# Performance work log

Hardware: AMD Instinct MI355X
Metric: run time of the kernel (lower is better)

## Reference

```python
import jax, jax.numpy as jnp
import numpy as np

N, K, D = 65536, 4096, 512
EPS_NORM = 1e-12
EPS_LOG = 1e-10


def _l2norm(x):
    # F.normalize(dim=-1): x / max(||x||, eps)
    n = jnp.sqrt(jnp.sum(x * x, axis=-1, keepdims=True))
    return x / jnp.maximum(n, EPS_NORM)


def setup_inputs() -> dict:
    key = jax.random.key(0)
    k1, k2, k3 = jax.random.split(key, 3)
    z_e = jax.random.normal(k1, (N, D), dtype=jnp.float32)
    embeddings = jax.random.normal(k2, (K, D), dtype=jnp.float32)
    logit_scale = jnp.ones((1,), dtype=jnp.float32) * 10.0
    residual_weight = jnp.asarray(0.3, dtype=jnp.float32)
    return {"z_e": z_e, "embeddings": embeddings,
            "logit_scale": logit_scale, "residual_weight": residual_weight}


def reference(z_e, embeddings, logit_scale, residual_weight):
    # cosine-similarity routing logits: [N, K]
    z_e_norm = _l2norm(z_e)
    emb_norm = _l2norm(embeddings)
    logits = logit_scale * jnp.einsum('nd,kd->nk', z_e_norm, emb_norm)

    # eval path (not training / not kmeans-initialized): hard argmax + gather
    indices = jnp.argmax(logits, axis=-1)          # [N] int
    z_q_pure = embeddings[indices]                 # [N, D]

    # learnable residual blend
    alpha = jax.nn.sigmoid(residual_weight)
    z_q = alpha * z_q_pure + (1.0 - alpha) * z_e

    # codebook usage perplexity
    probs = jax.nn.softmax(logits, axis=-1)        # [N, K]
    avg_probs = jnp.mean(probs, axis=0)            # [K]
    perplexity = jnp.exp(-jnp.sum(avg_probs * jnp.log(avg_probs + EPS_LOG)))

    return (z_q, indices, perplexity, alpha)
```

## Files before the change

### kernel.cpp

```cpp
#include <hip/hip_runtime.h>
#include <cstdint>
#include <cstddef>

#define N_ROWS 65536
#define K_CODES 4096
#define DIM 512
#define ND_OUT ((size_t)N_ROWS * DIM)

typedef __attribute__((ext_vector_type(8))) short  short8v;
typedef __attribute__((ext_vector_type(4))) float  f32x4;

#define WS_PACKED   0u
#define WS_SSUM     524288u
#define WS_AVGP     786432u
#define WS_ARN      802816u
#define WS_BRN      1064960u
#define WS_PLANES   2097152ull
#define SZ_APLANE   67108864ull
#define SZ_BPLANE   4194304ull
#define NEED_B      (WS_PLANES + 2*SZ_APLANE + 2*SZ_BPLANE)

#define PE_AH 0
#define PE_AL 33554432
#define PE_BH 67108864
#define PE_BL 69206016

#define GLOAD_LDS16(gsrc, ldst) \
  __builtin_amdgcn_global_load_lds((const __attribute__((address_space(1))) void*)(gsrc), \
                                   (__attribute__((address_space(3))) void*)(ldst), 16, 0, 0)

__device__ inline unsigned long long pack_max(float v, unsigned idx) {
    unsigned u = __float_as_uint(v);
    u = (u & 0x80000000u) ? ~u : (u | 0x80000000u);
    return ((unsigned long long)u << 32) | (unsigned)(~idx);
}

__device__ inline ushort bf16rn(float f) {
    unsigned u = __float_as_uint(f);
    u += 0x7FFFu + ((u >> 16) & 1u);
    return (ushort)(u >> 16);
}
__device__ inline float bf16f(ushort h) { return __uint_as_float((unsigned)h << 16); }


__global__ __launch_bounds__(256) void rownorm_kernel(const float* __restrict__ x,
                                                      float* __restrict__ out,
                                                      const float* __restrict__ scale_ptr) {
    int lane = threadIdx.x & 63;
    int row  = blockIdx.x * 4 + (threadIdx.x >> 6);
    const float4* x4 = reinterpret_cast<const float4*>(x) + (size_t)row * (DIM / 4);
    float4 v0 = x4[lane];
    float4 v1 = x4[64 + lane];
    float s = v0.x*v0.x + v0.y*v0.y + v0.z*v0.z + v0.w*v0.w
            + v1.x*v1.x + v1.y*v1.y + v1.z*v1.z + v1.w*v1.w;
#pragma unroll
    for (int off = 32; off; off >>= 1) s += __shfl_xor(s, off);
    if (lane == 0) {
        float scale = scale_ptr ? scale_ptr[0] : 1.0f;
        out[row] = scale / fmaxf(sqrtf(s), 1e-12f);
    }
}

__global__ __launch_bounds__(256) void split_bf16(const float* __restrict__ x,
                                                  ushort* __restrict__ hi,
                                                  ushort* __restrict__ lo, int n4) {
    int i = blockIdx.x * 256 + threadIdx.x;
    if (i >= n4) return;
    float4 v = reinterpret_cast<const float4*>(x)[i];
    ushort4 h, l;
    h.x = bf16rn(v.x); l.x = bf16rn(v.x - bf16f(h.x));
    h.y = bf16rn(v.y); l.y = bf16rn(v.y - bf16f(h.y));
    h.z = bf16rn(v.z); l.z = bf16rn(v.z - bf16f(h.z));
    h.w = bf16rn(v.w); l.w = bf16rn(v.w - bf16f(h.w));
    reinterpret_cast<ushort4*>(hi)[i] = h;
    reinterpret_cast<ushort4*>(lo)[i] = l;
}

template <int EPI, int TERMS>
__global__ __launch_bounds__(512, 2) void mfma2(
        const ushort* __restrict__ planes,
        const float* __restrict__ arn, const float* __restrict__ brn,
        unsigned long long* __restrict__ packed, float* __restrict__ ssum,
        float* __restrict__ avgp) {
    constexpr int BUFSZ = (TERMS == 4) ? 65536 : 32768;
    constexpr int BHOFF = (TERMS == 4) ? 32768 : 16384;
    constexpr int NST   = (TERMS == 4) ? 8 : 4;
    __shared__ __align__(16) char buf0[BUFSZ];
    __shared__ __align__(16) char buf1[BUFSZ];

    const int tid  = threadIdx.x;
    const int lane = tid & 63;
    const int wavei = __builtin_amdgcn_readfirstlane(tid >> 6);
    const int wr = wavei >> 1, wc = wavei & 1;
    const int r16 = lane & 15, kg = lane >> 4;

    const int orig = blockIdx.x;
    const int swz  = (orig & 7) * 512 + (orig >> 3);
    const int row0 = (swz >> 4) * 256, col0 = (swz & 15) * 256;

    const ushort* gsrc[NST];
    int ldsu[NST];
#pragma unroll
    for (int j = 0; j < NST; ++j) {
        int u = wavei * NST + j;
        int p = u >> 4, rb = u & 15;
        int pe, g0;
        if constexpr (TERMS == 4) {
            pe = (p == 0) ? PE_AH : (p == 1) ? PE_AL : (p == 2) ? PE_BH : PE_BL;
            g0 = (p < 2) ? row0 : col0;
        } else {
            pe = (p == 0) ? PE_AH : PE_BH;
            g0 = (p == 0) ? row0 : col0;
        }
        gsrc[j] = planes + pe + (size_t)(g0 + rb * 16 + r16) * DIM + kg * 8;
        ldsu[j] = u * 1024;
    }

    f32x4 acc[4][8];
#pragma unroll
    for (int m = 0; m < 4; ++m)
#pragma unroll
        for (int n = 0; n < 8; ++n) acc[m][n] = f32x4{0.f, 0.f, 0.f, 0.f};

#define MFMA_STEP(CUR, NXT, KT)                                                       \
    {                                                                                  \
        if ((KT) + 1 < 16) {                                                           \
            _Pragma("unroll")                                                          \
            for (int j = 0; j < NST; ++j)                                              \
                GLOAD_LDS16(gsrc[j] + ((KT) + 1) * 32, (char*)(NXT) + ldsu[j]);        \
        }                                                                              \
        short8v ah[4], al[4];                                                          \
        _Pragma("unroll")                                                              \
        for (int m = 0; m < 4; ++m) {                                                  \
            ah[m] = *(const short8v*)((CUR) + (wr * 4 + m) * 1024 + lane * 16);        \
            if constexpr (TERMS == 4)                                                  \
                al[m] = *(const short8v*)((CUR) + 16384 + (wr * 4 + m) * 1024 + lane * 16); \
        }                                                                              \
        __builtin_amdgcn_s_setprio(1);                                                 \
        _Pragma("unroll")                                                              \
        for (int nh = 0; nh < 2; ++nh) {                                               \
            short8v bh[4], bl[4];                                                      \
            _Pragma("unroll")                                                          \
            for (int n = 0; n < 4; ++n) {                                              \
                int nn = nh * 4 + n;                                                   \
                bh[n] = *(const short8v*)((CUR) + BHOFF + (wc * 8 + nn) * 1024 + lane * 16); \
                if constexpr (TERMS == 4)                                              \
                    bl[n] = *(const short8v*)((CUR) + 49152 + (wc * 8 + nn) * 1024 + lane * 16); \
            }                                                                          \
            _Pragma("unroll")                                                          \
            for (int m = 0; m < 4; ++m)                                                \
                _Pragma("unroll")                                                      \
                for (int n = 0; n < 4; ++n) {                                          \
                    int nn = nh * 4 + n;                                               \
                    acc[m][nn] = __builtin_amdgcn_mfma_f32_16x16x32_bf16(ah[m], bh[n], acc[m][nn], 0, 0, 0); \
                    if constexpr (TERMS == 4) {                                        \
                        acc[m][nn] = __builtin_amdgcn_mfma_f32_16x16x32_bf16(ah[m], bl[n], acc[m][nn], 0, 0, 0); \
                        acc[m][nn] = __builtin_amdgcn_mfma_f32_16x16x32_bf16(al[m], bh[n], acc[m][nn], 0, 0, 0); \
                        acc[m][nn] = __builtin_amdgcn_mfma_f32_16x16x32_bf16(al[m], bl[n], acc[m][nn], 0, 0, 0); \
                    }                                                                  \
                }                                                                      \
        }                                                                              \
        __builtin_amdgcn_s_setprio(0);                                                 \
        __syncthreads();                                                               \
    }

#pragma unroll
    for (int j = 0; j < NST; ++j)
        GLOAD_LDS16(gsrc[j], (char*)buf0 + ldsu[j]);
    __syncthreads();

#pragma unroll 1
    for (int kt = 0; kt < 16; kt += 2) {
        MFMA_STEP(buf0, buf1, kt);
        MFMA_STEP(buf1, buf0, kt + 1);
    }
#undef MFMA_STEP

    const int g = lane >> 4, c15 = lane & 15;
    float bc[8];
#pragma unroll
    for (int n = 0; n < 8; ++n) bc[n] = brn[col0 + wc * 128 + n * 16 + c15];

    if constexpr (EPI == 0) {
#pragma unroll
        for (int m = 0; m < 4; ++m)
#pragma unroll
            for (int rr = 0; rr < 4; ++rr) {
                const int grow = row0 + wr * 64 + m * 16 + g * 4 + rr;
                const float ar = arn[grow];
                float mx = -1e30f; int mi = 0; float se = 0.f;
#pragma unroll
                for (int n = 0; n < 8; ++n) {
                    float lg = acc[m][n][rr] * ar * bc[n];
                    int gcol = col0 + wc * 128 + n * 16 + c15;
                    se += __expf(lg);
                    if (lg > mx || (lg == mx && gcol < mi)) { mx = lg; mi = gcol; }
                }
#pragma unroll
                for (int off = 1; off < 16; off <<= 1) {
                    float om = __shfl_xor(mx, off, 16);
                    int   oi = __shfl_xor(mi, off, 16);
                    float os = __shfl_xor(se, off, 16);
                    se += os;
                    if (om > mx || (om == mx && oi < mi)) { mx = om; mi = oi; }
                }
                if (c15 == 0) {
                    atomicMax(packed + grow, pack_max(mx, (unsigned)mi));
                    atomicAdd(&ssum[grow], se);
                }
            }
    } else {
        float cp[8] = {0.f, 0.f, 0.f, 0.f, 0.f, 0.f, 0.f, 0.f};
#pragma unroll
        for (int m = 0; m < 4; ++m)
#pragma unroll
            for (int rr = 0; rr < 4; ++rr) {
                const int grow = row0 + wr * 64 + m * 16 + g * 4 + rr;
                const float ar = arn[grow];
                const float si = 1.0f / ssum[grow];
#pragma unroll
                for (int n = 0; n < 8; ++n)
                    cp[n] += __expf(acc[m][n][rr] * ar * bc[n]) * si;
            }
#pragma unroll
        for (int n = 0; n < 8; ++n) {
            cp[n] += __shfl_xor(cp[n], 16);
            cp[n] += __shfl_xor(cp[n], 32);
        }
        float* sm = (float*)buf0;
        if (g == 0) {
#pragma unroll
            for (int n = 0; n < 8; ++n) sm[wavei * 128 + n * 16 + c15] = cp[n];
        }
        __syncthreads();
        if (tid < 256) {
            int wcc = tid >> 7, j = tid & 127;
            float s = sm[(0 + wcc) * 128 + j] + sm[(2 + wcc) * 128 + j]
                    + sm[(4 + wcc) * 128 + j] + sm[(6 + wcc) * 128 + j];
            atomicAdd(&avgp[col0 + wcc * 128 + j], s);
        }
    }
}

template <int PASS>
__global__ __launch_bounds__(256) void gemm_pass(
        const float* __restrict__ A, const float* __restrict__ B,
        const float* __restrict__ arn, const float* __restrict__ brn,
        unsigned long long* __restrict__ packed, float* __restrict__ ssum,
        float* __restrict__ avgp) {
    __shared__ __align__(16) float As[16][132];
    __shared__ __align__(16) float Bs[16][132];
    const int tid = threadIdx.x;
    const int tr = tid >> 4, tc = tid & 15;
    const int row0 = blockIdx.y * 128, col0 = blockIdx.x * 128;

    float acc[8][8] = {};
    const float4* A4 = reinterpret_cast<const float4*>(A);
    const float4* B4 = reinterpret_cast<const float4*>(B);

    for (int d0 = 0; d0 < DIM; d0 += 16) {
#pragma unroll
        for (int l = 0; l < 2; ++l) {
            int q = tid + l * 256;
            int r = q >> 2, dq = q & 3;
            float4 av = A4[(size_t)(row0 + r) * (DIM / 4) + (d0 >> 2) + dq];
            float4 bv = B4[(size_t)(col0 + r) * (DIM / 4) + (d0 >> 2) + dq];
            As[dq*4+0][r] = av.x; As[dq*4+1][r] = av.y; As[dq*4+2][r] = av.z; As[dq*4+3][r] = av.w;
            Bs[dq*4+0][r] = bv.x; Bs[dq*4+1][r] = bv.y; Bs[dq*4+2][r] = bv.z; Bs[dq*4+3][r] = bv.w;
        }
        __syncthreads();
#pragma unroll
        for (int dd = 0; dd < 16; ++dd) {
            float4 a0 = *reinterpret_cast<const float4*>(&As[dd][tr * 4]);
            float4 a1 = *reinterpret_cast<const float4*>(&As[dd][64 + tr * 4]);
            float4 b0 = *reinterpret_cast<const float4*>(&Bs[dd][tc * 4]);
            float4 b1 = *reinterpret_cast<const float4*>(&Bs[dd][64 + tc * 4]);
            float av[8] = {a0.x, a0.y, a0.z, a0.w, a1.x, a1.y, a1.z, a1.w};
            float bv[8] = {b0.x, b0.y, b0.z, b0.w, b1.x, b1.y, b1.z, b1.w};
#pragma unroll
            for (int i = 0; i < 8; ++i)
#pragma unroll
                for (int j = 0; j < 8; ++j)
                    acc[i][j] = fmaf(av[i], bv[j], acc[i][j]);
        }
        __syncthreads();
    }

    int rows[8], cols[8];
    float ar[8], bcv[8];
#pragma unroll
    for (int i = 0; i < 8; ++i) {
        rows[i] = (i < 4) ? (tr * 4 + i) : (64 + tr * 4 + i - 4);
        ar[i] = arn[row0 + rows[i]];
    }
#pragma unroll
    for (int j = 0; j < 8; ++j) {
        cols[j] = (j < 4) ? (tc * 4 + j) : (64 + tc * 4 + j - 4);
        bcv[j] = brn[col0 + cols[j]];
    }

    if constexpr (PASS == 1) {
#pragma unroll
        for (int i = 0; i < 8; ++i) {
            float m = -1e30f; int mi = 0; float se = 0.0f;
#pragma unroll
            for (int j = 0; j < 8; ++j) {
                float l = acc[i][j] * ar[i] * bcv[j];
                int c = col0 + cols[j];
                if (l > m || (l == m && c < mi)) { m = l; mi = c; }
                se += expf(l);
            }
#pragma unroll
            for (int off = 1; off < 16; off <<= 1) {
                float om = __shfl_xor(m, off, 16);
                int   oi = __shfl_xor(mi, off, 16);
                float os = __shfl_xor(se, off, 16);
                se += os;
                if (om > m || (om == m && oi < mi)) { m = om; mi = oi; }
            }
            if (tc == 0) {
                int grow = row0 + rows[i];
                atomicMax(packed + grow, pack_max(m, (unsigned)mi));
                atomicAdd(&ssum[grow], se);
            }
        }
    } else {
        float sinv[8];
#pragma unroll
        for (int i = 0; i < 8; ++i) sinv[i] = 1.0f / ssum[row0 + rows[i]];
        float cp[8] = {};
#pragma unroll
        for (int i = 0; i < 8; ++i)
#pragma unroll
            for (int j = 0; j < 8; ++j)
                cp[j] += expf(acc[i][j] * ar[i] * bcv[j]) * sinv[i];
        __syncthreads();
        float* red = &As[0][0];
#pragma unroll
        for (int j = 0; j < 8; ++j) red[tr * 128 + cols[j]] = cp[j];
        __syncthreads();
        if (tid < 128) {
            float s = 0.0f;
#pragma unroll
            for (int t = 0; t < 16; ++t) s += red[t * 128 + tid];
            atomicAdd(&avgp[col0 + tid], s);
        }
    }
}

__global__ __launch_bounds__(256) void zq_kernel(const float* __restrict__ ze,
                                                 const float* __restrict__ emb,
                                                 const unsigned long long* __restrict__ packed,
                                                 const float* __restrict__ resw,
                                                 float* __restrict__ out) {
    int q = blockIdx.x * 256 + threadIdx.x;
    int n = q >> 7, d4 = q & 127;
    unsigned idx = ~(unsigned)(packed[n] & 0xFFFFFFFFull);
    float alpha = 1.0f / (1.0f + expf(-resw[0]));
    float4 e = reinterpret_cast<const float4*>(emb)[(size_t)idx * 128 + d4];
    float4 z = reinterpret_cast<const float4*>(ze)[(size_t)n * 128 + d4];
    float4 o;
    o.x = alpha * e.x + (1.0f - alpha) * z.x;
    o.y = alpha * e.y + (1.0f - alpha) * z.y;
    o.z = alpha * e.z + (1.0f - alpha) * z.z;
    o.w = alpha * e.w + (1.0f - alpha) * z.w;
    reinterpret_cast<float4*>(out)[(size_t)n * 128 + d4] = o;
    if (d4 == 0) out[ND_OUT + n] = (float)idx;
}

__global__ __launch_bounds__(256) void finalize_kernel(const float* __restrict__ avgp,
                                                       const float* __restrict__ resw,
                                                       float* __restrict__ out) {
    float acc = 0.0f;
    for (int k = threadIdx.x; k < K_CODES; k += 256) {
        float p = avgp[k] * (1.0f / (float)N_ROWS);
        acc += p * logf(p + 1e-10f);
    }
    __shared__ float red[4];
#pragma unroll
    for (int off = 32; off; off >>= 1) acc += __shfl_xor(acc, off);
    int lane = threadIdx.x & 63, wave = threadIdx.x >> 6;
    if (lane == 0) red[wave] = acc;
    __syncthreads();
    if (threadIdx.x == 0) {
        float s = red[0] + red[1] + red[2] + red[3];
        out[ND_OUT + N_ROWS]     = expf(-s);
        out[ND_OUT + N_ROWS + 1] = 1.0f / (1.0f + expf(-resw[0]));
    }
}

extern "C" void kernel_launch(void* const* d_in, const int* in_sizes, int n_in,
                              void* d_out, int out_size, void* d_ws, size_t ws_size,
                              hipStream_t stream) {
    const float* ze   = (const float*)d_in[0];
    const float* emb  = (const float*)d_in[1];
    const float* ls   = (const float*)d_in[2];
    const float* resw = (const float*)d_in[3];
    float* out = (float*)d_out;

    char* ws = (char*)d_ws;
    unsigned long long* packed = (unsigned long long*)(ws + WS_PACKED);
    float* ssum = (float*)(ws + WS_SSUM);
    float* avgp = (float*)(ws + WS_AVGP);
    float* arn  = (float*)(ws + WS_ARN);
    float* brn  = (float*)(ws + WS_BRN);

    hipMemsetAsync(d_ws, 0, 802816, stream);

    rownorm_kernel<<<N_ROWS / 4, 256, 0, stream>>>(ze, arn, ls);
    rownorm_kernel<<<K_CODES / 4, 256, 0, stream>>>(emb, brn, nullptr);

    if (ws_size >= NEED_B) {
        ushort* planes = (ushort*)(ws + WS_PLANES);
        split_bf16<<<(N_ROWS * DIM / 4) / 256, 256, 0, stream>>>(ze, planes + PE_AH, planes + PE_AL, N_ROWS * DIM / 4);
        split_bf16<<<(K_CODES * DIM / 4) / 256, 256, 0, stream>>>(emb, planes + PE_BH, planes + PE_BL, K_CODES * DIM / 4);

        mfma2<0, 4><<<4096, 512, 0, stream>>>(planes, arn, brn, packed, ssum, avgp);
        mfma2<2, 1><<<4096, 512, 0, stream>>>(planes, arn, brn, packed, ssum, avgp);
    } else {
        dim3 grid(K_CODES / 128, N_ROWS / 128);
        gemm_pass<1><<<grid, 256, 0, stream>>>(ze, emb, arn, brn, packed, ssum, avgp);
        gemm_pass<2><<<grid, 256, 0, stream>>>(ze, emb, arn, brn, packed, ssum, avgp);
    }

    zq_kernel<<<(N_ROWS * (DIM / 4)) / 256, 256, 0, stream>>>(ze, emb, packed, resw, out);
    finalize_kernel<<<1, 256, 0, stream>>>(avgp, resw, out);
}
```

Baseline: 1.514 ms.

## Restructure split-bf16 GEMM as 4-stage pipelined k-loop and fuse norm with split

The bf16 split GEMM now runs each hi/lo product combination as separate k-steps of a single-term MFMA loop. The loop uses a 4-slot LDS ring (128 KB) with explicit vmcnt waits and raw s_barrier, so global-to-LDS loads run two stages ahead instead of double buffering. The row-norm and bf16 hi/lo split kernels are fused so the inputs are read once. The larger LDS footprint may limit occupancy to one block per CU, and the explicit waitcnt choreography is fragile.

```diff
diff --git a/kernel.cpp b/kernel.cpp
--- a/kernel.cpp
+++ b/kernel.cpp
@@ -42,10 +42,11 @@
 }
 __device__ inline float bf16f(ushort h) { return __uint_as_float((unsigned)h << 16); }
 
-
-__global__ __launch_bounds__(256) void rownorm_kernel(const float* __restrict__ x,
-                                                      float* __restrict__ out,
-                                                      const float* __restrict__ scale_ptr) {
+__global__ __launch_bounds__(256) void norm_split(const float* __restrict__ x,
+                                                  ushort* __restrict__ hi,
+                                                  ushort* __restrict__ lo,
+                                                  float* __restrict__ nrm,
+                                                  const float* __restrict__ scale_ptr) {
     int lane = threadIdx.x & 63;
     int row  = blockIdx.x * 4 + (threadIdx.x >> 6);
     const float4* x4 = reinterpret_cast<const float4*>(x) + (size_t)row * (DIM / 4);
@@ -55,38 +56,35 @@
             + v1.x*v1.x + v1.y*v1.y + v1.z*v1.z + v1.w*v1.w;
 #pragma unroll
     for (int off = 32; off; off >>= 1) s += __shfl_xor(s, off);
+
+    ushort4 h0, l0, h1, l1;
+    h0.x = bf16rn(v0.x); l0.x = bf16rn(v0.x - bf16f(h0.x));
+    h0.y = bf16rn(v0.y); l0.y = bf16rn(v0.y - bf16f(h0.y));
+    h0.z = bf16rn(v0.z); l0.z = bf16rn(v0.z - bf16f(h0.z));
+    h0.w = bf16rn(v0.w); l0.w = bf16rn(v0.w - bf16f(h0.w));
+    h1.x = bf16rn(v1.x); l1.x = bf16rn(v1.x - bf16f(h1.x));
+    h1.y = bf16rn(v1.y); l1.y = bf16rn(v1.y - bf16f(h1.y));
+    h1.z = bf16rn(v1.z); l1.z = bf16rn(v1.z - bf16f(h1.z));
+    h1.w = bf16rn(v1.w); l1.w = bf16rn(v1.w - bf16f(h1.w));
+    ushort4* hi4 = reinterpret_cast<ushort4*>(hi) + (size_t)row * (DIM / 4);
+    ushort4* lo4 = reinterpret_cast<ushort4*>(lo) + (size_t)row * (DIM / 4);
+    hi4[lane] = h0; hi4[64 + lane] = h1;
+    lo4[lane] = l0; lo4[64 + lane] = l1;
+
     if (lane == 0) {
         float scale = scale_ptr ? scale_ptr[0] : 1.0f;
-        out[row] = scale / fmaxf(sqrtf(s), 1e-12f);
-    }
-}
-
-__global__ __launch_bounds__(256) void split_bf16(const float* __restrict__ x,
-                                                  ushort* __restrict__ hi,
-                                                  ushort* __restrict__ lo, int n4) {
-    int i = blockIdx.x * 256 + threadIdx.x;
-    if (i >= n4) return;
-    float4 v = reinterpret_cast<const float4*>(x)[i];
-    ushort4 h, l;
-    h.x = bf16rn(v.x); l.x = bf16rn(v.x - bf16f(h.x));
-    h.y = bf16rn(v.y); l.y = bf16rn(v.y - bf16f(h.y));
-    h.z = bf16rn(v.z); l.z = bf16rn(v.z - bf16f(h.z));
-    h.w = bf16rn(v.w); l.w = bf16rn(v.w - bf16f(h.w));
-    reinterpret_cast<ushort4*>(hi)[i] = h;
-    reinterpret_cast<ushort4*>(lo)[i] = l;
-}
-
-template <int EPI, int TERMS>
-__global__ __launch_bounds__(512, 2) void mfma2(
+        nrm[row] = scale / fmaxf(sqrtf(s), 1e-12f);
+    }
+}
+
+template <int EPI, int NREG>
+__global__ __launch_bounds__(512, 2) void mfma3(
         const ushort* __restrict__ planes,
         const float* __restrict__ arn, const float* __restrict__ brn,
         unsigned long long* __restrict__ packed, float* __restrict__ ssum,
         float* __restrict__ avgp) {
-    constexpr int BUFSZ = (TERMS == 4) ? 65536 : 32768;
-    constexpr int BHOFF = (TERMS == 4) ? 32768 : 16384;
-    constexpr int NST   = (TERMS == 4) ? 8 : 4;
-    __shared__ __align__(16) char buf0[BUFSZ];
-    __shared__ __align__(16) char buf1[BUFSZ];
+    constexpr int NSTEPS = NREG * 16;
+    __shared__ __align__(16) char lds[131072];
 
     const int tid  = threadIdx.x;
     const int lane = tid & 63;
@@ -98,23 +96,30 @@
     const int swz  = (orig & 7) * 512 + (orig >> 3);
     const int row0 = (swz >> 4) * 256, col0 = (swz & 15) * 256;
 
-    const ushort* gsrc[NST];
-    int ldsu[NST];
-#pragma unroll
-    for (int j = 0; j < NST; ++j) {
-        int u = wavei * NST + j;
-        int p = u >> 4, rb = u & 15;
-        int pe, g0;
-        if constexpr (TERMS == 4) {
-            pe = (p == 0) ? PE_AH : (p == 1) ? PE_AL : (p == 2) ? PE_BH : PE_BL;
-            g0 = (p < 2) ? row0 : col0;
-        } else {
-            pe = (p == 0) ? PE_AH : PE_BH;
-            g0 = (p == 0) ? row0 : col0;
-        }
-        gsrc[j] = planes + pe + (size_t)(g0 + rb * 16 + r16) * DIM + kg * 8;
-        ldsu[j] = u * 1024;
-    }
+    size_t rowoff[4];
+    int ldso[4];
+    bool uA[4];
+#pragma unroll
+    for (int j = 0; j < 4; ++j) {
+        int u = wavei * 4 + j;
+        bool a = (u < 16);
+        int g0 = a ? row0 : col0;
+        rowoff[j] = (size_t)(g0 + (u & 15) * 16 + r16) * DIM + kg * 8;
+        ldso[j] = u * 1024;
+        uA[j] = a;
+    }
+
+    auto STAGE = [&](int ks, char* slot) {
+        int rg  = (ks >> 4) & 3;
+        int kk  = (ks & 15) * 32;
+        int bA = (rg & 1) ? PE_AL : PE_AH;
+        int bB = ((rg ^ (rg >> 1)) & 1) ? PE_BL : PE_BH;
+#pragma unroll
+        for (int j = 0; j < 4; ++j) {
+            const ushort* src = planes + (uA[j] ? bA : bB) + kk + rowoff[j];
+            GLOAD_LDS16(src, slot + ldso[j]);
+        }
+    };
 
     f32x4 acc[4][8];
 #pragma unroll
@@ -122,59 +127,54 @@
 #pragma unroll
         for (int n = 0; n < 8; ++n) acc[m][n] = f32x4{0.f, 0.f, 0.f, 0.f};
 
-#define MFMA_STEP(CUR, NXT, KT)                                                       \
-    {                                                                                  \
-        if ((KT) + 1 < 16) {                                                           \
-            _Pragma("unroll")                                                          \
-            for (int j = 0; j < NST; ++j)                                              \
-                GLOAD_LDS16(gsrc[j] + ((KT) + 1) * 32, (char*)(NXT) + ldsu[j]);        \
-        }                                                                              \
-        short8v ah[4], al[4];                                                          \
-        _Pragma("unroll")                                                              \
-        for (int m = 0; m < 4; ++m) {                                                  \
-            ah[m] = *(const short8v*)((CUR) + (wr * 4 + m) * 1024 + lane * 16);        \
-            if constexpr (TERMS == 4)                                                  \
-                al[m] = *(const short8v*)((CUR) + 16384 + (wr * 4 + m) * 1024 + lane * 16); \
-        }                                                                              \
-        __builtin_amdgcn_s_setprio(1);                                                 \
-        _Pragma("unroll")                                                              \
-        for (int nh = 0; nh < 2; ++nh) {                                               \
-            short8v bh[4], bl[4];                                                      \
-            _Pragma("unroll")                                                          \
-            for (int n = 0; n < 4; ++n) {                                              \
-                int nn = nh * 4 + n;                                                   \
-                bh[n] = *(const short8v*)((CUR) + BHOFF + (wc * 8 + nn) * 1024 + lane * 16); \
-                if constexpr (TERMS == 4)                                              \
-                    bl[n] = *(const short8v*)((CUR) + 49152 + (wc * 8 + nn) * 1024 + lane * 16); \
-            }                                                                          \
-            _Pragma("unroll")                                                          \
-            for (int m = 0; m < 4; ++m)                                                \
-                _Pragma("unroll")                                                      \
-                for (int n = 0; n < 4; ++n) {                                          \
-                    int nn = nh * 4 + n;                                               \
-                    acc[m][nn] = __builtin_amdgcn_mfma_f32_16x16x32_bf16(ah[m], bh[n], acc[m][nn], 0, 0, 0); \
-                    if constexpr (TERMS == 4) {                                        \
-                        acc[m][nn] = __builtin_amdgcn_mfma_f32_16x16x32_bf16(ah[m], bl[n], acc[m][nn], 0, 0, 0); \
-                        acc[m][nn] = __builtin_amdgcn_mfma_f32_16x16x32_bf16(al[m], bh[n], acc[m][nn], 0, 0, 0); \
-                        acc[m][nn] = __builtin_amdgcn_mfma_f32_16x16x32_bf16(al[m], bl[n], acc[m][nn], 0, 0, 0); \
-                    }                                                                  \
-                }                                                                      \
-        }                                                                              \
-        __builtin_amdgcn_s_setprio(0);                                                 \
-        __syncthreads();                                                               \
-    }
-
-#pragma unroll
-    for (int j = 0; j < NST; ++j)
-        GLOAD_LDS16(gsrc[j], (char*)buf0 + ldsu[j]);
-    __syncthreads();
+    char* const S0 = lds;
+    char* const S1 = lds + 32768;
+    char* const S2 = lds + 65536;
+    char* const S3 = lds + 98304;
+
+#define KSTEP(CUR, NXT, KS, DO_STAGE, VMC)                                              \
+    do {                                                                                \
+        short8v a_[4], b_[8];                                                           \
+        _Pragma("unroll")                                                               \
+        for (int m = 0; m < 4; ++m)                                                     \
+            a_[m] = *(const short8v*)((CUR) + (wr * 4 + m) * 1024 + lane * 16);         \
+        _Pragma("unroll")                                                               \
+        for (int n = 0; n < 8; ++n)                                                     \
+            b_[n] = *(const short8v*)((CUR) + 16384 + (wc * 8 + n) * 1024 + lane * 16); \
+        asm volatile("s_waitcnt lgkmcnt(0)" ::: "memory");                              \
+        if (DO_STAGE) STAGE((KS), (NXT));                                               \
+        asm volatile("s_waitcnt vmcnt(" #VMC ")" ::: "memory");                         \
+        asm volatile("s_barrier" ::: "memory");                                         \
+        __builtin_amdgcn_sched_barrier(0);                                              \
+        __builtin_amdgcn_s_setprio(1);                                                  \
+        _Pragma("unroll")                                                               \
+        for (int m = 0; m < 4; ++m)                                                     \
+            _Pragma("unroll")                                                           \
+            for (int n = 0; n < 8; ++n)                                                 \
+                acc[m][n] = __builtin_amdgcn_mfma_f32_16x16x32_bf16(a_[m], b_[n],       \
+                                                                    acc[m][n], 0, 0, 0);\
+        __builtin_amdgcn_s_setprio(0);                                                  \
+        __builtin_amdgcn_sched_barrier(0);                                              \
+    } while (0)
+
+    STAGE(0, S0);
+    STAGE(1, S1);
+    asm volatile("s_waitcnt vmcnt(4)" ::: "memory");
+    asm volatile("s_barrier" ::: "memory");
+    __builtin_amdgcn_sched_barrier(0);
 
 #pragma unroll 1
-    for (int kt = 0; kt < 16; kt += 2) {
-        MFMA_STEP(buf0, buf1, kt);
-        MFMA_STEP(buf1, buf0, kt + 1);
-    }
-#undef MFMA_STEP
+    for (int kt0 = 0; kt0 < NSTEPS - 4; kt0 += 4) {
+        KSTEP(S0, S2, kt0 + 2, true, 4);
+        KSTEP(S1, S3, kt0 + 3, true, 4);
+        KSTEP(S2, S0, kt0 + 4, true, 4);
+        KSTEP(S3, S1, kt0 + 5, true, 4);
+    }
+    KSTEP(S0, S2, NSTEPS - 2, true, 4);
+    KSTEP(S1, S3, NSTEPS - 1, true, 4);
+    KSTEP(S2, S0, 0, false, 0);
+    KSTEP(S3, S0, 0, false, 0);
+#undef KSTEP
 
     const int g = lane >> 4, c15 = lane & 15;
     float bc[8];
@@ -227,7 +227,7 @@
             cp[n] += __shfl_xor(cp[n], 16);
             cp[n] += __shfl_xor(cp[n], 32);
         }
-        float* sm = (float*)buf0;
+        float* sm = (float*)lds;
         if (g == 0) {
 #pragma unroll
             for (int n = 0; n < 8; ++n) sm[wavei * 128 + n * 16 + c15] = cp[n];
@@ -407,22 +407,43 @@
 
     hipMemsetAsync(d_ws, 0, 802816, stream);
 
-    rownorm_kernel<<<N_ROWS / 4, 256, 0, stream>>>(ze, arn, ls);
-    rownorm_kernel<<<K_CODES / 4, 256, 0, stream>>>(emb, brn, nullptr);
-
     if (ws_size >= NEED_B) {
         ushort* planes = (ushort*)(ws + WS_PLANES);
-        split_bf16<<<(N_ROWS * DIM / 4) / 256, 256, 0, stream>>>(ze, planes + PE_AH, planes + PE_AL, N_ROWS * DIM / 4);
-        split_bf16<<<(K_CODES * DIM / 4) / 256, 256, 0, stream>>>(emb, planes + PE_BH, planes + PE_BL, K_CODES * DIM / 4);
-
-        mfma2<0, 4><<<4096, 512, 0, stream>>>(planes, arn, brn, packed, ssum, avgp);
-        mfma2<2, 1><<<4096, 512, 0, stream>>>(planes, arn, brn, packed, ssum, avgp);
+        norm_split<<<N_ROWS / 4, 256, 0, stream>>>(ze, planes + PE_AH, planes + PE_AL, arn, ls);
+        norm_split<<<K_CODES / 4, 256, 0, stream>>>(emb, planes + PE_BH, planes + PE_BL, brn, nullptr);
+
+        mfma3<0, 4><<<4096, 512, 0, stream>>>(planes, arn, brn, packed, ssum, avgp);
+        mfma3<2, 1><<<4096, 512, 0, stream>>>(planes, arn, brn, packed, ssum, avgp);
     } else {
+        float* arn2 = arn; float* brn2 = brn;
+        {
+        }
+        extern __global__ void rownorm_only(const float*, float*, const float*);
+        rownorm_only<<<N_ROWS / 4, 256, 0, stream>>>(ze, arn2, ls);
+        rownorm_only<<<K_CODES / 4, 256, 0, stream>>>(emb, brn2, nullptr);
         dim3 grid(K_CODES / 128, N_ROWS / 128);
-        gemm_pass<1><<<grid, 256, 0, stream>>>(ze, emb, arn, brn, packed, ssum, avgp);
-        gemm_pass<2><<<grid, 256, 0, stream>>>(ze, emb, arn, brn, packed, ssum, avgp);
+        gemm_pass<1><<<grid, 256, 0, stream>>>(ze, emb, arn2, brn2, packed, ssum, avgp);
+        gemm_pass<2><<<grid, 256, 0, stream>>>(ze, emb, arn2, brn2, packed, ssum, avgp);
     }
 
     zq_kernel<<<(N_ROWS * (DIM / 4)) / 256, 256, 0, stream>>>(ze, emb, packed, resw, out);
     finalize_kernel<<<1, 256, 0, stream>>>(avgp, resw, out);
 }
+
+__global__ __launch_bounds__(256) void rownorm_only(const float* __restrict__ x,
+                                                    float* __restrict__ outp,
+                                                    const float* __restrict__ scale_ptr) {
+    int lane = threadIdx.x & 63;
+    int row  = blockIdx.x * 4 + (threadIdx.x >> 6);
+    const float4* x4 = reinterpret_cast<const float4*>(x) + (size_t)row * (DIM / 4);
+    float4 v0 = x4[lane];
+    float4 v1 = x4[64 + lane];
+    float s = v0.x*v0.x + v0.y*v0.y + v0.z*v0.z + v0.w*v0.w
+            + v1.x*v1.x + v1.y*v1.y + v1.z*v1.z + v1.w*v1.w;
+#pragma unroll
+    for (int off = 32; off; off >>= 1) s += __shfl_xor(s, off);
+    if (lane == 0) {
+        float scale = scale_ptr ? scale_ptr[0] : 1.0f;
+        outp[row] = scale / fmaxf(sqrtf(s), 1e-12f);
+    }
+}
```

Result: slower. 1.730 ms (+14.3%).
